# Performance work log

Measured on AMD Instinct MI355X. Metric: run time of the kernel, lower is better.

The kernel has to match this reference:

```python
import jax, jax.numpy as jnp
import numpy as np

D = 256  # feature_dim
NQ = 512
NK = 512


def setup_inputs() -> dict:
    key = jax.random.key(0)
    ks = jax.random.split(key, 12)
    s = 0.05
    return {
        "x": jax.random.normal(ks[0], (1, D, NQ), dtype=jnp.float32),
        "source": jax.random.normal(ks[1], (1, D, NK), dtype=jnp.float32),
        "dist": jax.random.normal(ks[2], (1, D, NQ * NK), dtype=jnp.float32),
        "mask": jax.random.randint(ks[3], (NQ, NK), 0, 2).astype(jnp.bool_),
        # MLPAttention mlp: channels [3D, D, 1] (1x1 convs == per-position matmuls)
        "aW1": jax.random.normal(ks[4], (D, 3 * D), dtype=jnp.float32) * s,
        "ab1": jax.random.normal(ks[5], (D,), dtype=jnp.float32) * s,
        "aW2": jax.random.normal(ks[6], (1, D), dtype=jnp.float32) * s,
        "ab2": jax.random.normal(ks[7], (1,), dtype=jnp.float32) * s,
        # merge mlp: channels [2D, 2D, D], last bias initialized to 0
        "mW1": jax.random.normal(ks[8], (2 * D, 2 * D), dtype=jnp.float32) * s,
        "mb1": jax.random.normal(ks[9], (2 * D,), dtype=jnp.float32) * s,
        "mW2": jax.random.normal(ks[10], (D, 2 * D), dtype=jnp.float32) * s,
        "mb2": jnp.zeros((D,), dtype=jnp.float32),
    }


def _conv1x1(W, b, x):
    # Conv1d(kernel_size=1): (out,in) @ (b,in,n) -> (b,out,n)
    return jnp.einsum('oc,bcn->bon', W, x) + b[None, :, None]


def reference(x, source, dist, mask, aW1, ab1, aW2, ab2, mW1, mb1, mW2, mb2):
    nq, nk = x.shape[-1], source.shape[-1]
    d = x.shape[1]
    # broadcast query over keys and key over queries, flatten to (1, d, nq*nk)
    qb = jnp.broadcast_to(x[:, :, :, None], (1, d, nq, nk)).reshape(1, d, nq * nk)
    kb = jnp.broadcast_to(source[:, :, None, :], (1, d, nq, nk)).reshape(1, d, nq * nk)
    feat = jnp.concatenate([qb, kb, dist], axis=1)  # (1, 3d, nq*nk)
    h = jax.nn.relu(_conv1x1(aW1, ab1, feat))       # (1, d, nq*nk)
    scores = _conv1x1(aW2, ab2, h).reshape(1, nq, nk)
    # boolean-mask branch: push masked-out entries far below the min
    neg = jax.lax.stop_gradient(scores.min()) - 20.0
    scores = scores + neg * (~mask).astype(scores.dtype)[None]
    prob = jax.nn.softmax(scores, axis=-1)
    message = jnp.einsum('bnm,bdm->bdn', prob, source)  # value == source
    # merge MLP on concat([x, message])
    cat = jnp.concatenate([x, message], axis=1)  # (1, 2d, nq)
    h2 = jax.nn.relu(_conv1x1(mW1, mb1, cat))
    out = _conv1x1(mW2, mb2, h2)  # (1, d, nq)
    return (out, scores)
```

## Files before the change

kernel.cpp:

```cpp
#include <hip/hip_runtime.h>
#include <stdint.h>

#define D_ 256
#define NQ_ 512
#define NK_ 512
#define NP_ (NQ_*NK_)

typedef __attribute__((ext_vector_type(8))) __bf16 bf16x8;
typedef __attribute__((ext_vector_type(4))) float f32x4;

__device__ __forceinline__ unsigned short f2bf(float f) {
  unsigned u = __builtin_bit_cast(unsigned, f);
  u += 0x7FFFu + ((u >> 16) & 1u);
  return (unsigned short)(u >> 16);
}
__device__ __forceinline__ unsigned encf(float f) {
  unsigned u = __builtin_bit_cast(unsigned, f);
  return (u & 0x80000000u) ? ~u : (u | 0x80000000u);
}
__device__ __forceinline__ float decf(unsigned e) {
  unsigned u = (e & 0x80000000u) ? (e ^ 0x80000000u) : ~e;
  return __builtin_bit_cast(float, u);
}

template<int EPI, int KTILES>
__device__ __forceinline__ void gemm_body(
    const unsigned short* __restrict__ A, int lda,
    const unsigned short* __restrict__ B, int ldb,
    const float* __restrict__ bias,
    void* __restrict__ Dst, int ldd, int nTilesN, int bid) {
  const int t = threadIdx.x, w = t >> 6, l = t & 63, l15 = l & 15, g = l >> 4;
  const int bm = bid / nTilesN, bn = bid % nTilesN;
  const int m0 = bm*64 + w*16, n0 = bn*64;
  const unsigned short* Ap = A + (size_t)(m0 + l15)*lda + g*8;
  const unsigned short* Bp = B + (size_t)(n0 + l15)*ldb + g*8;
  f32x4 acc[4];
  #pragma unroll
  for (int n = 0; n < 4; ++n) acc[n] = (f32x4){0.f,0.f,0.f,0.f};
  #pragma unroll 2
  for (int kk = 0; kk < KTILES; ++kk) {
    bf16x8 a = *(const bf16x8*)(Ap + kk*32);
    #pragma unroll
    for (int n = 0; n < 4; ++n) {
      bf16x8 b = *(const bf16x8*)(Bp + (size_t)n*16*ldb + kk*32);
      acc[n] = __builtin_amdgcn_mfma_f32_16x16x32_bf16(a, b, acc[n], 0, 0, 0);
    }
  }
  #pragma unroll
  for (int n = 0; n < 4; ++n) {
    const int col = n0 + n*16 + l15;
    const float bc = (EPI & 4) ? bias[col] : 0.f;
    #pragma unroll
    for (int r = 0; r < 4; ++r) {
      const int m = m0 + g*4 + r;
      float v = acc[n][r] + bc;
      if (EPI & 8) v += bias[m];
      if (EPI & 2) v = fmaxf(v, 0.f);
      if (EPI & 1) ((unsigned short*)Dst)[(size_t)m*ldd + col] = f2bf(v);
      else         ((float*)Dst)[(size_t)m*ldd + col] = v;
    }
  }
}

template<int EPI, int KTILES>
__global__ __launch_bounds__(256) void gemm_k(
    const unsigned short* __restrict__ A, int lda,
    const unsigned short* __restrict__ B, int ldb,
    const float* __restrict__ bias,
    void* __restrict__ Dst, int ldd, int nTilesN) {
  gemm_body<EPI, KTILES>(A, lda, B, ldb, bias, Dst, ldd, nTilesN, blockIdx.x);
}

__global__ __launch_bounds__(256) void kprep(
    const unsigned* __restrict__ maskw, unsigned* __restrict__ wsMin,
    unsigned* __restrict__ wsFlag,
    const float* __restrict__ aW1, const float* __restrict__ source,
    const float* __restrict__ x, const float* __restrict__ mW1,
    const float* __restrict__ mW2,
    unsigned short* __restrict__ Cb, unsigned short* __restrict__ srcbf,
    unsigned short* __restrict__ mW1b, unsigned short* __restrict__ mW2b,
    unsigned short* __restrict__ aW1A, unsigned short* __restrict__ aW1B,
    unsigned short* __restrict__ catT, unsigned short* __restrict__ srcT) {
  __shared__ float tile[64][65];
  const int b = blockIdx.x, t = threadIdx.x;
  if (b == 0) {
    if (t < 64) {
      unsigned a01 = 1, af = 1;
      for (int i = 0; i < 4; ++i) {
        unsigned v = maskw[t*4 + i];
        a01 &= (v == 0u || v == 1u) ? 1u : 0u;
        af  &= (v == 0u || v == 0x3f800000u) ? 1u : 0u;
      }
      unsigned long long b01 = __ballot(a01 != 0), bf = __ballot(af != 0);
      if (t == 0) {
        *wsFlag = (b01 == ~0ull) ? 1u : ((bf == ~0ull) ? 2u : 0u);
        *wsMin = 0xFFFFFFFFu;
      }
    }
    return;
  }
  if (b < 705) {
    const int bb = b - 1;
    const float* src; unsigned short* dst;
    if (bb < 64)        { int j = bb*1024 + t*4;       int e=j>>8, c=j&255; src = aW1 + e*768 + 512 + c; dst = Cb + j; }
    else if (bb < 192)  { int j = (bb-64)*1024 + t*4;  src = source + j;    dst = srcbf + j; }
    else if (bb < 448)  { int j = (bb-192)*1024 + t*4; src = mW1 + j;       dst = mW1b + j; }
    else if (bb < 576)  { int j = (bb-448)*1024 + t*4; src = mW2 + j;       dst = mW2b + j; }
    else if (bb < 640)  { int j = (bb-576)*1024 + t*4; int e=j>>8, c=j&255; src = aW1 + e*768 + c;       dst = aW1A + j; }
    else                { int j = (bb-640)*1024 + t*4; int e=j>>8, c=j&255; src = aW1 + e*768 + 256 + c; dst = aW1B + j; }
    const float4 v = *(const float4*)src;
    ushort4 o; o.x=f2bf(v.x); o.y=f2bf(v.y); o.z=f2bf(v.z); o.w=f2bf(v.w);
    *(ushort4*)dst = o;
    return;
  }
  const float* src; unsigned short* dst; int ldd, bid;
  if (b < 737) { src = x;      dst = catT; ldd = 512; bid = b - 705; }
  else         { src = source; dst = srcT; ldd = 256; bid = b - 737; }
  const int bd = bid >> 3, bq = bid & 7;
  const int r = t >> 4, c4 = (t & 15) * 4;
  #pragma unroll
  for (int rr = 0; rr < 4; ++rr) {
    int dl = rr*16 + r;
    float4 v = *(const float4*)(src + (size_t)(bd*64 + dl)*512 + bq*64 + c4);
    tile[dl][c4+0] = v.x; tile[dl][c4+1] = v.y; tile[dl][c4+2] = v.z; tile[dl][c4+3] = v.w;
  }
  __syncthreads();
  #pragma unroll
  for (int rr = 0; rr < 4; ++rr) {
    int j = rr*16 + r;
    ushort4 o;
    o.x = f2bf(tile[c4+0][j]); o.y = f2bf(tile[c4+1][j]);
    o.z = f2bf(tile[c4+2][j]); o.w = f2bf(tile[c4+3][j]);
    *(ushort4*)(dst + (size_t)(bq*64 + j)*ldd + bd*64 + c4) = o;
  }
}

__global__ __launch_bounds__(256) void kprep2(
    const unsigned short* __restrict__ catT, const unsigned short* __restrict__ aW1A,
    const float* __restrict__ ab1, float* __restrict__ Up,
    const unsigned short* __restrict__ aW1B, const unsigned short* __restrict__ srcT,
    float* __restrict__ Vm) {
  if (blockIdx.x < 32)
    gemm_body<4, 8>(catT, 512, aW1A, 256, ab1, (void*)Up, 256, 4, blockIdx.x);
  else
    gemm_body<0, 8>(aW1B, 256, srcT, 256, (const float*)nullptr, (void*)Vm, 512, 8, blockIdx.x - 32);
}

__global__ __launch_bounds__(256) void kscores(
    const float* __restrict__ dist, const unsigned short* __restrict__ Cb,
    const float* __restrict__ Up, const float* __restrict__ Vm,
    const float* __restrict__ aW2, const float* __restrict__ ab2,
    float* __restrict__ outScores, unsigned* __restrict__ wsMin) {
  __shared__ __align__(16) unsigned char ldsB[2][64*256];
  __shared__ float u_s[256], aw2_s[256];
  __shared__ float red[4][64];

  const int t = threadIdx.x;
  const int w = t >> 6;
  const int l = t & 63;
  const int l15 = l & 15;
  const int g = l >> 4;

  const int p0 = blockIdx.x * 64;
  const int q  = p0 >> 9;
  const int k0 = p0 & 511;

  const int quad1 = (w + g) & 3;
  const int quad2 = quad1 + 4;

  float st[64];
  const float* dbase = dist + (size_t)p0 + l;
  #pragma unroll
  for (int kk = 0; kk < 8; ++kk) {
    #pragma unroll
    for (int i = 0; i < 4; ++i) {
      st[kk*8 + i]     = dbase[(size_t)(kk*32 + quad1*4 + i) * NP_];
      st[kk*8 + 4 + i] = dbase[(size_t)(kk*32 + quad2*4 + i) * NP_];
    }
  }

  u_s[t]   = Up[q*256 + t];
  aw2_s[t] = aW2[t];

  f32x4 acc[4][4];
  #pragma unroll
  for (int m = 0; m < 4; ++m)
    #pragma unroll
    for (int n = 0; n < 4; ++n) acc[m][n] = (f32x4){0.f, 0.f, 0.f, 0.f};

  const unsigned short* Abase = Cb + (size_t)(w*64 + l15)*256 + g*8;

  #pragma unroll
  for (int h = 0; h < 2; ++h) {
    #pragma unroll
    for (int kk2 = 0; kk2 < 4; ++kk2) {
      const int kk = h*4 + kk2;
      {
        const int c0 = kk2*32 + quad1*4;
        unsigned lo = (unsigned)f2bf(st[kk*8+0]) | ((unsigned)f2bf(st[kk*8+1]) << 16);
        unsigned hi = (unsigned)f2bf(st[kk*8+2]) | ((unsigned)f2bf(st[kk*8+3]) << 16);
        *(uint2*)(&ldsB[h][l*256 + (((c0>>3) ^ (l&7)) << 4) + ((c0>>2)&1)*8]) = make_uint2(lo, hi);
      }
      {
        const int c0 = kk2*32 + quad2*4;
        unsigned lo = (unsigned)f2bf(st[kk*8+4]) | ((unsigned)f2bf(st[kk*8+5]) << 16);
        unsigned hi = (unsigned)f2bf(st[kk*8+6]) | ((unsigned)f2bf(st[kk*8+7]) << 16);
        *(uint2*)(&ldsB[h][l*256 + (((c0>>3) ^ (l&7)) << 4) + ((c0>>2)&1)*8]) = make_uint2(lo, hi);
      }
    }
    __syncthreads();
    #pragma unroll
    for (int kk2 = 0; kk2 < 4; ++kk2) {
      const int kk = h*4 + kk2;
      bf16x8 a[4], bfrag[4];
      #pragma unroll
      for (int m = 0; m < 4; ++m)
        a[m] = *(const bf16x8*)(Abase + (size_t)m*16*256 + kk*32);
      #pragma unroll
      for (int n = 0; n < 4; ++n) {
        const int j = n*16 + l15;
        const int c0 = kk2*32 + g*8;
        bfrag[n] = *(const bf16x8*)(&ldsB[h][j*256 + (((c0>>3) ^ (j&7)) << 4)]);
      }
      #pragma unroll
      for (int m = 0; m < 4; ++m)
        #pragma unroll
        for (int n = 0; n < 4; ++n)
          acc[m][n] = __builtin_amdgcn_mfma_f32_16x16x32_bf16(a[m], bfrag[n], acc[m][n], 0, 0, 0);
    }
  }

  float part[4];
  #pragma unroll
  for (int n = 0; n < 4; ++n) {
    int j = k0 + n*16 + l15;
    float s = 0.f;
    #pragma unroll
    for (int m = 0; m < 4; ++m) {
      #pragma unroll
      for (int r = 0; r < 4; ++r) {
        int e = w*64 + m*16 + g*4 + r;
        float gv = acc[m][n][r] + u_s[e] + Vm[e*512 + j];
        s += aw2_s[e] * fmaxf(gv, 0.f);
      }
    }
    s += __shfl_xor(s, 16);
    s += __shfl_xor(s, 32);
    part[n] = s;
  }
  if (l < 16) {
    #pragma unroll
    for (int n = 0; n < 4; ++n) red[w][n*16 + l] = part[n];
  }
  __syncthreads();
  if (t < 64) {
    float s = red[0][t] + red[1][t] + red[2][t] + red[3][t] + ab2[0];
    outScores[p0 + t] = s;
    float mn = s;
    #pragma unroll
    for (int off = 32; off; off >>= 1) mn = fminf(mn, __shfl_xor(mn, off));
    if (t == 0) atomicMin(wsMin, encf(mn));
  }
}

__global__ __launch_bounds__(256) void ksoftmax(
    const void* __restrict__ maskp,
    const unsigned* __restrict__ wsMin, const unsigned* __restrict__ wsFlag,
    float* __restrict__ scores, unsigned short* __restrict__ prob) {
  __shared__ float srow[512];
  __shared__ float redl[8];
  const int t = threadIdx.x, w = t >> 6, l = t & 63;
  const int q = blockIdx.x;
  const float neg = decf(*wsMin) - 20.0f;
  const unsigned flag = *wsFlag;

  for (int k = t; k < 512; k += 256) {
    float raw = scores[q*512 + k];
    bool mv;
    if (flag == 1)      mv = ((const int*)maskp)[q*512 + k] != 0;
    else if (flag == 2) mv = ((const float*)maskp)[q*512 + k] != 0.f;
    else                mv = ((const unsigned char*)maskp)[q*512 + k] != 0;
    float ms = raw + (mv ? 0.f : neg);
    scores[q*512 + k] = ms;
    srow[k] = ms;
  }
  __syncthreads();
  float lm = fmaxf(srow[t], srow[t + 256]);
  #pragma unroll
  for (int off = 32; off; off >>= 1) lm = fmaxf(lm, __shfl_xor(lm, off));
  if (l == 0) redl[w] = lm;
  __syncthreads();
  float rmax = fmaxf(fmaxf(redl[0], redl[1]), fmaxf(redl[2], redl[3]));
  float e0 = __expf(srow[t] - rmax), e1 = __expf(srow[t + 256] - rmax);
  float ls = e0 + e1;
  #pragma unroll
  for (int off = 32; off; off >>= 1) ls += __shfl_xor(ls, off);
  if (l == 0) redl[4 + w] = ls;
  __syncthreads();
  float inv = 1.0f / (redl[4] + redl[5] + redl[6] + redl[7]);
  prob[q*512 + t]       = f2bf(e0 * inv);
  prob[q*512 + t + 256] = f2bf(e1 * inv);
}

extern "C" void kernel_launch(void* const* d_in, const int* in_sizes, int n_in,
                              void* d_out, int out_size, void* d_ws, size_t ws_size,
                              hipStream_t stream) {
  const float* x      = (const float*)d_in[0];
  const float* source = (const float*)d_in[1];
  const float* dist   = (const float*)d_in[2];
  const void*  mask   = (const void*)d_in[3];
  const float* aW1    = (const float*)d_in[4];
  const float* ab1    = (const float*)d_in[5];
  const float* aW2    = (const float*)d_in[6];
  const float* ab2    = (const float*)d_in[7];
  const float* mW1    = (const float*)d_in[8];
  const float* mb1    = (const float*)d_in[9];
  const float* mW2    = (const float*)d_in[10];
  const float* mb2    = (const float*)d_in[11];

  float* outMain = (float*)d_out;
  float* scores  = outMain + 256*512;

  char* ws = (char*)d_ws;
  unsigned* wsMin  = (unsigned*)ws;
  unsigned* wsFlag = wsMin + 1;
  unsigned short* Cb    = (unsigned short*)(ws + 1024);
  float*          Up    = (float*)(ws + 132096);
  float*          Vm    = (float*)(ws + 656384);
  unsigned short* srcbf = (unsigned short*)(ws + 1180672);
  unsigned short* srcT  = (unsigned short*)(ws + 1442816);
  unsigned short* mW1b  = (unsigned short*)(ws + 1704960);
  unsigned short* mW2b  = (unsigned short*)(ws + 2229248);
  unsigned short* aW1A  = (unsigned short*)(ws + 2491392);
  unsigned short* aW1B  = (unsigned short*)(ws + 2622464);
  unsigned short* catT  = (unsigned short*)(ws + 2753536);
  unsigned short* prob  = (unsigned short*)(ws + 3277824);
  unsigned short* h2T   = (unsigned short*)(ws + 3802112);

  hipLaunchKernelGGL(kprep, dim3(769), dim3(256), 0, stream,
                     (const unsigned*)mask, wsMin, wsFlag, aW1, source, x, mW1, mW2,
                     Cb, srcbf, mW1b, mW2b, aW1A, aW1B, catT, srcT);
  hipLaunchKernelGGL(kprep2, dim3(64), dim3(256), 0, stream,
                     catT, aW1A, ab1, Up, aW1B, srcT, Vm);
  hipLaunchKernelGGL(kscores, dim3(4096), dim3(256), 0, stream,
                     dist, Cb, Up, Vm, aW2, ab2, scores, wsMin);
  hipLaunchKernelGGL(ksoftmax, dim3(512), dim3(256), 0, stream,
                     mask, wsMin, wsFlag, scores, prob);
  hipLaunchKernelGGL((gemm_k<1, 16>), dim3(32), dim3(256), 0, stream,
                     prob, 512, srcbf, 512, (const float*)nullptr, (void*)(catT + 256), 512, 4);
  hipLaunchKernelGGL((gemm_k<7, 16>), dim3(64), dim3(256), 0, stream,
                     catT, 512, mW1b, 512, mb1, (void*)h2T, 512, 8);
  hipLaunchKernelGGL((gemm_k<8, 16>), dim3(32), dim3(256), 0, stream,
                     mW2b, 512, h2T, 512, mb2, (void*)outMain, 512, 8);
}
```

Baseline: 177.8 us.

## Make kscores persistent per query row with register-prefetched dist tiles

The scores kernel now runs one block per query row (512 blocks instead of 4096). Each block loops over eight 64-key tiles, prefetching the next tile's dist values into registers with float4 loads while the MFMA work on the current tile runs. The LDS layout switches to a single 256-channel buffer with a new XOR swizzle. The row minimum is reduced locally, so there is one atomic per row, and launch bounds request 2 blocks per SM. The aim is to hide global-load latency on the large dist stream and cut per-block setup, at the cost of fewer blocks in flight and higher register pressure.

```diff
diff --git a/kernel.cpp b/kernel.cpp
--- a/kernel.cpp
+++ b/kernel.cpp
@@ -146,12 +146,12 @@
     gemm_body<0, 8>(aW1B, 256, srcT, 256, (const float*)nullptr, (void*)Vm, 512, 8, blockIdx.x - 32);
 }
 
-__global__ __launch_bounds__(256) void kscores(
+__global__ __launch_bounds__(256, 2) void kscores(
     const float* __restrict__ dist, const unsigned short* __restrict__ Cb,
     const float* __restrict__ Up, const float* __restrict__ Vm,
     const float* __restrict__ aW2, const float* __restrict__ ab2,
     float* __restrict__ outScores, unsigned* __restrict__ wsMin) {
-  __shared__ __align__(16) unsigned char ldsB[2][64*256];
+  __shared__ __align__(16) unsigned char ldsB[64*512];
   __shared__ float u_s[256], aw2_s[256];
   __shared__ float red[4][64];
 
@@ -160,67 +160,57 @@
   const int l = t & 63;
   const int l15 = l & 15;
   const int g = l >> 4;
-
-  const int p0 = blockIdx.x * 64;
-  const int q  = p0 >> 9;
-  const int k0 = p0 & 511;
-
-  const int quad1 = (w + g) & 3;
-  const int quad2 = quad1 + 4;
-
-  float st[64];
-  const float* dbase = dist + (size_t)p0 + l;
-  #pragma unroll
-  for (int kk = 0; kk < 8; ++kk) {
-    #pragma unroll
-    for (int i = 0; i < 4; ++i) {
-      st[kk*8 + i]     = dbase[(size_t)(kk*32 + quad1*4 + i) * NP_];
-      st[kk*8 + 4 + i] = dbase[(size_t)(kk*32 + quad2*4 + i) * NP_];
-    }
-  }
+  const int q = blockIdx.x;
 
   u_s[t]   = Up[q*256 + t];
   aw2_s[t] = aW2[t];
 
-  f32x4 acc[4][4];
-  #pragma unroll
-  for (int m = 0; m < 4; ++m)
-    #pragma unroll
-    for (int n = 0; n < 4; ++n) acc[m][n] = (f32x4){0.f, 0.f, 0.f, 0.f};
-
+  const float* dbase = dist + (size_t)(w*64 + g)*NP_ + q*512 + 4*l15;
   const unsigned short* Abase = Cb + (size_t)(w*64 + l15)*256 + g*8;
 
-  #pragma unroll
-  for (int h = 0; h < 2; ++h) {
-    #pragma unroll
-    for (int kk2 = 0; kk2 < 4; ++kk2) {
-      const int kk = h*4 + kk2;
-      {
-        const int c0 = kk2*32 + quad1*4;
-        unsigned lo = (unsigned)f2bf(st[kk*8+0]) | ((unsigned)f2bf(st[kk*8+1]) << 16);
-        unsigned hi = (unsigned)f2bf(st[kk*8+2]) | ((unsigned)f2bf(st[kk*8+3]) << 16);
-        *(uint2*)(&ldsB[h][l*256 + (((c0>>3) ^ (l&7)) << 4) + ((c0>>2)&1)*8]) = make_uint2(lo, hi);
-      }
-      {
-        const int c0 = kk2*32 + quad2*4;
-        unsigned lo = (unsigned)f2bf(st[kk*8+4]) | ((unsigned)f2bf(st[kk*8+5]) << 16);
-        unsigned hi = (unsigned)f2bf(st[kk*8+6]) | ((unsigned)f2bf(st[kk*8+7]) << 16);
-        *(uint2*)(&ldsB[h][l*256 + (((c0>>3) ^ (l&7)) << 4) + ((c0>>2)&1)*8]) = make_uint2(lo, hi);
+  float4 v[16];
+  #pragma unroll
+  for (int i = 0; i < 16; ++i)
+    v[i] = *(const float4*)(dbase + (size_t)(i*4)*NP_);
+
+  float rowmin = 1e30f;
+
+  for (int tt = 0; tt < 8; ++tt) {
+    #pragma unroll
+    for (int i = 0; i < 16; ++i) {
+      const int c  = w*64 + i*4 + g;
+      const int C3 = c >> 3, c7 = c & 7;
+      #pragma unroll
+      for (int r = 0; r < 4; ++r) {
+        const int p = 4*l15 + r;
+        const int chunk = C3 ^ (l15 ^ (r << 2));
+        *(unsigned short*)(&ldsB[p*512 + chunk*16 + c7*2]) =
+            f2bf(((const float*)&v[i])[r]);
       }
     }
     __syncthreads();
-    #pragma unroll
-    for (int kk2 = 0; kk2 < 4; ++kk2) {
-      const int kk = h*4 + kk2;
+    if (tt < 7) {
+      #pragma unroll
+      for (int i = 0; i < 16; ++i)
+        v[i] = *(const float4*)(dbase + (size_t)(i*4)*NP_ + (tt+1)*64);
+    }
+    f32x4 acc[4][4];
+    #pragma unroll
+    for (int m = 0; m < 4; ++m)
+      #pragma unroll
+      for (int n = 0; n < 4; ++n) acc[m][n] = (f32x4){0.f, 0.f, 0.f, 0.f};
+    #pragma unroll
+    for (int kk = 0; kk < 8; ++kk) {
       bf16x8 a[4], bfrag[4];
       #pragma unroll
       for (int m = 0; m < 4; ++m)
         a[m] = *(const bf16x8*)(Abase + (size_t)m*16*256 + kk*32);
       #pragma unroll
       for (int n = 0; n < 4; ++n) {
-        const int j = n*16 + l15;
-        const int c0 = kk2*32 + g*8;
-        bfrag[n] = *(const bf16x8*)(&ldsB[h][j*256 + (((c0>>3) ^ (j&7)) << 4)]);
+        const int p = n*16 + l15;
+        const int S = ((p >> 2) ^ ((p & 3) << 2)) & 15;
+        const int chunk = (kk*4 + g) ^ S;
+        bfrag[n] = *(const bf16x8*)(&ldsB[p*512 + chunk*16]);
       }
       #pragma unroll
       for (int m = 0; m < 4; ++m)
@@ -228,38 +218,40 @@
         for (int n = 0; n < 4; ++n)
           acc[m][n] = __builtin_amdgcn_mfma_f32_16x16x32_bf16(a[m], bfrag[n], acc[m][n], 0, 0, 0);
     }
-  }
-
-  float part[4];
-  #pragma unroll
-  for (int n = 0; n < 4; ++n) {
-    int j = k0 + n*16 + l15;
-    float s = 0.f;
-    #pragma unroll
-    for (int m = 0; m < 4; ++m) {
-      #pragma unroll
-      for (int r = 0; r < 4; ++r) {
-        int e = w*64 + m*16 + g*4 + r;
-        float gv = acc[m][n][r] + u_s[e] + Vm[e*512 + j];
-        s += aw2_s[e] * fmaxf(gv, 0.f);
-      }
-    }
-    s += __shfl_xor(s, 16);
-    s += __shfl_xor(s, 32);
-    part[n] = s;
-  }
-  if (l < 16) {
-    #pragma unroll
-    for (int n = 0; n < 4; ++n) red[w][n*16 + l] = part[n];
-  }
-  __syncthreads();
+
+    float part[4];
+    #pragma unroll
+    for (int n = 0; n < 4; ++n) {
+      const int j = tt*64 + n*16 + l15;
+      float s = 0.f;
+      #pragma unroll
+      for (int m = 0; m < 4; ++m) {
+        #pragma unroll
+        for (int r = 0; r < 4; ++r) {
+          const int e = w*64 + m*16 + g*4 + r;
+          float gv = acc[m][n][r] + u_s[e] + Vm[e*512 + j];
+          s += aw2_s[e] * fmaxf(gv, 0.f);
+        }
+      }
+      s += __shfl_xor(s, 16);
+      s += __shfl_xor(s, 32);
+      part[n] = s;
+    }
+    if (l < 16) {
+      #pragma unroll
+      for (int n = 0; n < 4; ++n) red[w][n*16 + l] = part[n];
+    }
+    __syncthreads();
+    if (t < 64) {
+      float s = red[0][t] + red[1][t] + red[2][t] + red[3][t] + ab2[0];
+      outScores[q*512 + tt*64 + t] = s;
+      rowmin = fminf(rowmin, s);
+    }
+  }
   if (t < 64) {
-    float s = red[0][t] + red[1][t] + red[2][t] + red[3][t] + ab2[0];
-    outScores[p0 + t] = s;
-    float mn = s;
-    #pragma unroll
-    for (int off = 32; off; off >>= 1) mn = fminf(mn, __shfl_xor(mn, off));
-    if (t == 0) atomicMin(wsMin, encf(mn));
+    #pragma unroll
+    for (int off = 32; off; off >>= 1) rowmin = fminf(rowmin, __shfl_xor(rowmin, off));
+    if (t == 0) atomicMin(wsMin, encf(rowmin));
   }
 }
 
@@ -342,7 +334,7 @@
                      Cb, srcbf, mW1b, mW2b, aW1A, aW1B, catT, srcT);
   hipLaunchKernelGGL(kprep2, dim3(64), dim3(256), 0, stream,
                      catT, aW1A, ab1, Up, aW1B, srcT, Vm);
-  hipLaunchKernelGGL(kscores, dim3(4096), dim3(256), 0, stream,
+  hipLaunchKernelGGL(kscores, dim3(512), dim3(256), 0, stream,
                      dist, Cb, Up, Vm, aW2, ab2, scores, wsMin);
   hipLaunchKernelGGL(ksoftmax, dim3(512), dim3(256), 0, stream,
                      mask, wsMin, wsFlag, scores, prob);
```

After: 282.2 us. 58.7% more time.

## Software-pipeline dist loads in kscores with double-buffered small LDS tiles

Applied to the files above, without the earlier changes.

Instead of loading all 64 dist values per thread into registers up front, the scores kernel now streams the K dimension in 8 steps. It prefetches two steps ahead into register buffers and double-buffers a much smaller LDS tile, so global loads overlap with MFMA compute. Register and LDS use drop, and launch bounds now request 3 blocks per CU for higher occupancy. Blocks are also remapped so consecutive block IDs stride across queries, which changes the memory access order; the cost is more barriers (one per step instead of two total).

```diff
diff --git a/kernel.cpp b/kernel.cpp
--- a/kernel.cpp
+++ b/kernel.cpp
@@ -146,12 +146,53 @@
     gemm_body<0, 8>(aW1B, 256, srcT, 256, (const float*)nullptr, (void*)Vm, 512, 8, blockIdx.x - 32);
 }
 
-__global__ __launch_bounds__(256) void kscores(
+__device__ __forceinline__ void loads8(float (&s)[8], const float* __restrict__ dbase,
+                                       int kk, int quad1, int quad2) {
+  #pragma unroll
+  for (int i = 0; i < 4; ++i) s[i]   = dbase[(size_t)(kk*32 + quad1*4 + i) * NP_];
+  #pragma unroll
+  for (int i = 0; i < 4; ++i) s[4+i] = dbase[(size_t)(kk*32 + quad2*4 + i) * NP_];
+}
+__device__ __forceinline__ void cvtwrite(unsigned char* __restrict__ buf, const float (&s)[8],
+                                         int l, int quad1, int quad2) {
+  const int key = (l >> 1) & 3;
+  {
+    unsigned lo = (unsigned)f2bf(s[0]) | ((unsigned)f2bf(s[1]) << 16);
+    unsigned hi = (unsigned)f2bf(s[2]) | ((unsigned)f2bf(s[3]) << 16);
+    *(uint2*)(buf + l*64 + ((((quad1>>1) ^ key) << 4) | ((quad1 & 1) << 3))) = make_uint2(lo, hi);
+  }
+  {
+    unsigned lo = (unsigned)f2bf(s[4]) | ((unsigned)f2bf(s[5]) << 16);
+    unsigned hi = (unsigned)f2bf(s[6]) | ((unsigned)f2bf(s[7]) << 16);
+    *(uint2*)(buf + l*64 + ((((quad2>>1) ^ key) << 4) | ((quad2 & 1) << 3))) = make_uint2(lo, hi);
+  }
+}
+__device__ __forceinline__ void computeStep(f32x4 (&acc)[4][4],
+                                            const unsigned short* __restrict__ Abase,
+                                            const unsigned char* __restrict__ buf,
+                                            int kk, int l15, int g) {
+  bf16x8 a[4], bfrag[4];
+  #pragma unroll
+  for (int m = 0; m < 4; ++m)
+    a[m] = *(const bf16x8*)(Abase + (size_t)m*16*256 + kk*32);
+  #pragma unroll
+  for (int n = 0; n < 4; ++n) {
+    const int p = n*16 + l15;
+    bfrag[n] = *(const bf16x8*)(buf + p*64 + ((g ^ ((p >> 1) & 3)) << 4));
+  }
+  #pragma unroll
+  for (int m = 0; m < 4; ++m)
+    #pragma unroll
+    for (int n = 0; n < 4; ++n)
+      acc[m][n] = __builtin_amdgcn_mfma_f32_16x16x32_bf16(a[m], bfrag[n], acc[m][n], 0, 0, 0);
+}
+
+__global__ __launch_bounds__(256, 3) void kscores(
     const float* __restrict__ dist, const unsigned short* __restrict__ Cb,
     const float* __restrict__ Up, const float* __restrict__ Vm,
     const float* __restrict__ aW2, const float* __restrict__ ab2,
     float* __restrict__ outScores, unsigned* __restrict__ wsMin) {
-  __shared__ __align__(16) unsigned char ldsB[2][64*256];
+  __shared__ __align__(16) unsigned char ldsB[2][64*64];
   __shared__ float u_s[256], aw2_s[256];
   __shared__ float red[4][64];
 
@@ -161,23 +202,20 @@
   const int l15 = l & 15;
   const int g = l >> 4;
 
-  const int p0 = blockIdx.x * 64;
+  const int bid = blockIdx.x;
+  const int p0 = ((bid & 7) * 512 + (bid >> 3)) * 64;
   const int q  = p0 >> 9;
   const int k0 = p0 & 511;
 
   const int quad1 = (w + g) & 3;
   const int quad2 = quad1 + 4;
 
-  float st[64];
   const float* dbase = dist + (size_t)p0 + l;
-  #pragma unroll
-  for (int kk = 0; kk < 8; ++kk) {
-    #pragma unroll
-    for (int i = 0; i < 4; ++i) {
-      st[kk*8 + i]     = dbase[(size_t)(kk*32 + quad1*4 + i) * NP_];
-      st[kk*8 + 4 + i] = dbase[(size_t)(kk*32 + quad2*4 + i) * NP_];
-    }
-  }
+  const unsigned short* Abase = Cb + (size_t)(w*64 + l15)*256 + g*8;
+
+  float sA[8], sB[8];
+  loads8(sA, dbase, 0, quad1, quad2);
+  loads8(sB, dbase, 1, quad1, quad2);
 
   u_s[t]   = Up[q*256 + t];
   aw2_s[t] = aW2[t];
@@ -188,46 +226,22 @@
     #pragma unroll
     for (int n = 0; n < 4; ++n) acc[m][n] = (f32x4){0.f, 0.f, 0.f, 0.f};
 
-  const unsigned short* Abase = Cb + (size_t)(w*64 + l15)*256 + g*8;
-
-  #pragma unroll
-  for (int h = 0; h < 2; ++h) {
-    #pragma unroll
-    for (int kk2 = 0; kk2 < 4; ++kk2) {
-      const int kk = h*4 + kk2;
-      {
-        const int c0 = kk2*32 + quad1*4;
-        unsigned lo = (unsigned)f2bf(st[kk*8+0]) | ((unsigned)f2bf(st[kk*8+1]) << 16);
-        unsigned hi = (unsigned)f2bf(st[kk*8+2]) | ((unsigned)f2bf(st[kk*8+3]) << 16);
-        *(uint2*)(&ldsB[h][l*256 + (((c0>>3) ^ (l&7)) << 4) + ((c0>>2)&1)*8]) = make_uint2(lo, hi);
-      }
-      {
-        const int c0 = kk2*32 + quad2*4;
-        unsigned lo = (unsigned)f2bf(st[kk*8+4]) | ((unsigned)f2bf(st[kk*8+5]) << 16);
-        unsigned hi = (unsigned)f2bf(st[kk*8+6]) | ((unsigned)f2bf(st[kk*8+7]) << 16);
-        *(uint2*)(&ldsB[h][l*256 + (((c0>>3) ^ (l&7)) << 4) + ((c0>>2)&1)*8]) = make_uint2(lo, hi);
-      }
+  cvtwrite(ldsB[0], sA, l, quad1, quad2);
+  __syncthreads();
+
+  #pragma unroll
+  for (int kk = 0; kk < 8; ++kk) {
+    const int b = kk & 1;
+    if (kk < 6) {
+      if (b == 0) loads8(sA, dbase, kk + 2, quad1, quad2);
+      else        loads8(sB, dbase, kk + 2, quad1, quad2);
+    }
+    computeStep(acc, Abase, ldsB[b], kk, l15, g);
+    if (kk < 7) {
+      if (b == 0) cvtwrite(ldsB[1], sB, l, quad1, quad2);
+      else        cvtwrite(ldsB[0], sA, l, quad1, quad2);
     }
     __syncthreads();
-    #pragma unroll
-    for (int kk2 = 0; kk2 < 4; ++kk2) {
-      const int kk = h*4 + kk2;
-      bf16x8 a[4], bfrag[4];
-      #pragma unroll
-      for (int m = 0; m < 4; ++m)
-        a[m] = *(const bf16x8*)(Abase + (size_t)m*16*256 + kk*32);
-      #pragma unroll
-      for (int n = 0; n < 4; ++n) {
-        const int j = n*16 + l15;
-        const int c0 = kk2*32 + g*8;
-        bfrag[n] = *(const bf16x8*)(&ldsB[h][j*256 + (((c0>>3) ^ (j&7)) << 4)]);
-      }
-      #pragma unroll
-      for (int m = 0; m < 4; ++m)
-        #pragma unroll
-        for (int n = 0; n < 4; ++n)
-          acc[m][n] = __builtin_amdgcn_mfma_f32_16x16x32_bf16(a[m], bfrag[n], acc[m][n], 0, 0, 0);
-    }
   }
 
   float part[4];
```

Result: slower. 186.5 us (+4.9%).
